# Kernel tuning notes

Hardware: AMD Instinct MI355X
Metric: run time of the kernel (lower is better)

The kernel has to match this reference:

```python
import jax, jax.numpy as jnp
import numpy as np

K = 512   # per-head dim == input dim
H = 8     # heads

def setup_inputs() -> dict:
    key = jax.random.key(0)
    ks = jax.random.split(key, 6)
    b, t = 4, 2048
    x = jax.random.normal(ks[0], (b, t, K), dtype=jnp.float32)
    s = 0.02
    Wq = jax.random.normal(ks[1], (K, K * H), dtype=jnp.float32) * s
    Wk = jax.random.normal(ks[2], (K, K * H), dtype=jnp.float32) * s
    Wv = jax.random.normal(ks[3], (K, K * H), dtype=jnp.float32) * s
    Wo = jax.random.normal(ks[4], (K * H, K), dtype=jnp.float32) * s
    bo = jnp.zeros((K,), dtype=jnp.float32)
    return {"x": x, "Wq": Wq, "Wk": Wk, "Wv": Wv, "Wo": Wo, "bo": bo}

def reference(x, Wq, Wk, Wv, Wo, bo):
    b, t, _ = x.shape
    scale = K ** 0.25
    # rearrange 'b t (k h) -> (b h) t k' == reshape (b,t,K,H) then move h next to b
    def split_heads(y):
        return y.reshape(b, t, K, H).transpose(0, 3, 1, 2)  # [b,h,t,K]
    q = split_heads(x @ Wq) / scale
    k_ = split_heads(x @ Wk) / scale
    v = split_heads(x @ Wv)
    dot = jnp.einsum('bhtk,bhsk->bhts', q, k_)      # [b,h,t,t]
    attn = jax.nn.softmax(dot, axis=-1)
    o = jnp.einsum('bhts,bhsk->bhtk', attn, v)      # [b,h,t,K]
    # '(b h) t k -> b t (h k)': heads outer in concat
    o = o.transpose(0, 2, 1, 3).reshape(b, t, H * K)
    return o @ Wo + bo
```

## Files before the change

kernel.cpp:

```cpp
#include <hip/hip_runtime.h>

typedef unsigned short u16;
typedef unsigned char u8;
typedef unsigned int u32;
typedef long i64;
typedef __attribute__((ext_vector_type(8))) short bf16x8;
typedef __attribute__((ext_vector_type(4))) float f32x4;
typedef __attribute__((ext_vector_type(16))) float f32x16;
typedef __attribute__((ext_vector_type(4))) u16 u16x4;
typedef __attribute__((ext_vector_type(4))) u32 u32x4;

__device__ __forceinline__ u16 f2bf(float f) {
  u32 u = __builtin_bit_cast(u32, f);
  return (u16)((u + 0x7FFFu + ((u >> 16) & 1u)) >> 16);
}
__device__ __forceinline__ u8 f2fp8(float f) {
  int w = __builtin_amdgcn_cvt_pk_fp8_f32(f, 0.f, 0, false);
  return (u8)(w & 0xff);
}

__device__ __forceinline__ f32x4 mfma16(bf16x8 a, bf16x8 b, f32x4 c) {
  return __builtin_amdgcn_mfma_f32_16x16x32_bf16(a, b, c, 0, 0, 0);
}
__device__ __forceinline__ f32x16 mfma32(bf16x8 a, bf16x8 b, f32x16 c) {
  return __builtin_amdgcn_mfma_f32_32x32x16_bf16(a, b, c, 0, 0, 0);
}
__device__ __forceinline__ f32x16 mfma32f8(i64 a, i64 b, f32x16 c) {
  return __builtin_amdgcn_mfma_f32_32x32x16_fp8_fp8(a, b, c, 0, 0, 0);
}

__device__ __forceinline__ void gload16(const void* g, void* l) {
  __builtin_amdgcn_global_load_lds(
      (const __attribute__((address_space(1))) unsigned int*)g,
      (__attribute__((address_space(3))) unsigned int*)l, 16, 0, 0);
}

__device__ __forceinline__ u32 cvtpk(float lo, float hi) {
  u32 r;
  asm volatile("v_cvt_pk_bf16_f32 %0, %1, %2" : "=v"(r) : "v"(lo), "v"(hi));
  return r;
}
__device__ __forceinline__ void pl32swap(u32& a, u32& b) {
  asm volatile("v_permlane32_swap_b32 %0, %1" : "+v"(a), "+v"(b));
}


__global__ void pack_x_kernel(const float* __restrict__ x, u16* __restrict__ xb) {
  const int i = blockIdx.x * 256 + threadIdx.x;
  const float4 v = ((const float4*)x)[i];
  u16x4 o;
  o[0] = f2bf(v.x); o[1] = f2bf(v.y); o[2] = f2bf(v.z); o[3] = f2bf(v.w);
  ((u16x4*)xb)[i] = o;
}

__global__ void pack_wqkv_t(const float* __restrict__ W, u16* __restrict__ Wp) {
  __shared__ u16 tile[64][72];
  const int t = threadIdx.x;
  const int c0 = blockIdx.x * 64, dd0 = blockIdx.y * 64;
#pragma unroll
  for (int s = 0; s < 4; ++s) {
    const int r = s * 16 + (t >> 4);
    const int q = (t & 15) * 4;
    const float4 v = *(const float4*)&W[(size_t)(dd0 + r) * 4096 + c0 + q];
    tile[r][q + 0] = f2bf(v.x); tile[r][q + 1] = f2bf(v.y);
    tile[r][q + 2] = f2bf(v.z); tile[r][q + 3] = f2bf(v.w);
  }
  __syncthreads();
#pragma unroll
  for (int s = 0; s < 4; ++s) {
    const int cl = s * 16 + (t >> 4);
    const int u = t & 15;
    const int cg = c0 + cl;
    const int orow = (cg & 7) * 512 + (cg >> 3);
    u16x4 o;
#pragma unroll
    for (int i = 0; i < 4; ++i) o[i] = tile[u * 4 + i][cl];
    *(u16x4*)&Wp[(size_t)orow * 512 + dd0 + u * 4] = o;
  }
}

__global__ void pack_wo_t(const float* __restrict__ W, u16* __restrict__ Wp) {
  __shared__ u16 tile[64][72];
  const int t = threadIdx.x;
  const int k0 = blockIdx.x * 64, n0 = blockIdx.y * 64;
#pragma unroll
  for (int s = 0; s < 4; ++s) {
    const int r = s * 16 + (t >> 4);
    const int q = (t & 15) * 4;
    const float4 v = *(const float4*)&W[(size_t)(k0 + r) * 512 + n0 + q];
    tile[r][q + 0] = f2bf(v.x); tile[r][q + 1] = f2bf(v.y);
    tile[r][q + 2] = f2bf(v.z); tile[r][q + 3] = f2bf(v.w);
  }
  __syncthreads();
#pragma unroll
  for (int s = 0; s < 4; ++s) {
    const int cl = s * 16 + (t >> 4);
    const int u = t & 15;
    u16x4 o;
#pragma unroll
    for (int i = 0; i < 4; ++i) o[i] = tile[u * 4 + i][cl];
    *(u16x4*)&Wp[(size_t)(n0 + cl) * 4096 + k0 + u * 4] = o;
  }
}


template <int MODE>
__global__ __launch_bounds__(256, 2) void gemm_bf16(
    const u16* __restrict__ A, const u16* __restrict__ B,
    void* __restrict__ Cout, const float* __restrict__ bias,
    int Kd, float scale) {
  __shared__ u16 Al[128 * 64];
  __shared__ u16 Bl[128 * 64];
  const int tid = threadIdx.x;
  const int lane = tid & 63;
  const int w = tid >> 6, wm = w >> 1, wn = w & 1;
  const int l15 = lane & 15, lg = lane >> 4;
  const int m0 = blockIdx.y * 128, n0 = blockIdx.x * 128;

  f32x4 acc[4][4];
  const f32x4 zero = {0.f, 0.f, 0.f, 0.f};
#pragma unroll
  for (int i = 0; i < 4; ++i)
#pragma unroll
    for (int j = 0; j < 4; ++j) acc[i][j] = zero;

  const int nk = Kd >> 6;
  for (int kt = 0; kt < nk; ++kt) {
    __syncthreads();
    const int k0 = kt << 6;
#pragma unroll
    for (int s = 0; s < 4; ++s) {
      const int chunk = s * 256 + tid;
      const int row = chunk >> 3, c = chunk & 7;
      const int cs = c ^ (row & 7);
      gload16(A + (size_t)(m0 + row) * Kd + k0 + cs * 8, &Al[chunk * 8]);
    }
#pragma unroll
    for (int s = 0; s < 4; ++s) {
      const int chunk = s * 256 + tid;
      const int row = chunk >> 3, c = chunk & 7;
      const int cs = c ^ (row & 7);
      gload16(B + (size_t)(n0 + row) * Kd + k0 + cs * 8, &Bl[chunk * 8]);
    }
    __syncthreads();
#pragma unroll
    for (int kk = 0; kk < 2; ++kk) {
      bf16x8 af[4], bfr[4];
      const int ch = kk * 4 + lg;
#pragma unroll
      for (int i = 0; i < 4; ++i) {
        const int ar = wm * 64 + i * 16 + l15;
        af[i] = *(const bf16x8*)&Al[ar * 64 + ((ch ^ (ar & 7)) * 8)];
        const int br = wn * 64 + i * 16 + l15;
        bfr[i] = *(const bf16x8*)&Bl[br * 64 + ((ch ^ (br & 7)) * 8)];
      }
#pragma unroll
      for (int i = 0; i < 4; ++i)
#pragma unroll
        for (int j = 0; j < 4; ++j)
          acc[i][j] = mfma16(af[i], bfr[j], acc[i][j]);
    }
  }

#pragma unroll
  for (int i = 0; i < 4; ++i) {
    const int gr0 = m0 + wm * 64 + i * 16 + lg * 4;
#pragma unroll
    for (int j = 0; j < 4; ++j) {
      const int gc = n0 + wn * 64 + j * 16 + l15;
      if constexpr (MODE == 0) {
        u8* O = (u8*)Cout;
        const int h = gc >> 9, d = gc & 511;
#pragma unroll
        for (int r = 0; r < 4; ++r) {
          const int grr = gr0 + r;
          const int bb = grr >> 11, t = grr & 2047;
          O[((size_t)((bb * 8 + h) * 2048 + t) << 9) + d] = f2fp8(acc[i][j][r] * scale);
        }
      } else if constexpr (MODE == 1) {
        u16* O = (u16*)Cout;
        const int h = gc >> 9, d = gc & 511;
        const int bb = gr0 >> 11, t = gr0 & 2047;
        u16x4 pk;
#pragma unroll
        for (int r = 0; r < 4; ++r) pk[r] = f2bf(acc[i][j][r]);
        *(u16x4*)&O[((size_t)((bb * 8 + h) * 512 + d) << 11) + t] = pk;
      } else {
        float* O = (float*)Cout;
        const float bv = bias[gc];
#pragma unroll
        for (int r = 0; r < 4; ++r)
          O[(size_t)(gr0 + r) * 512 + gc] = acc[i][j][r] + bv;
      }
    }
  }
}


__global__ __launch_bounds__(512, 2) void attn_kernel(
    const u8* __restrict__ Qg, const u8* __restrict__ Kg,
    const u16* __restrict__ Vtg, u16* __restrict__ Og, int nbh_pxcd) {
  __shared__ u8 K8[2][32 * 512];
  __shared__ u16 Vt_lds[2][512 * 32];
  __shared__ float Sxf[8][32][32];

  const int tid = threadIdx.x;
  const int lane = tid & 63;
  const int w = tid >> 6;
  const int pr = w >> 1, whalf = w & 1;
  const int l31 = lane & 31, hi = lane >> 5;

  const int bid = blockIdx.x;
  const int x8 = bid & 7, rest = bid >> 3;
  const int qt = rest & 15;
  const int bh = x8 * nbh_pxcd + (rest >> 4);

  const u8* Qb = Qg + (size_t)bh * 2048 * 512;
  const u8* Kb = Kg + (size_t)bh * 2048 * 512;
  const u16* Vb = Vtg + (size_t)bh * 2048 * 512;

  const int qrow = qt * 128 + pr * 32 + l31;
  i64 qf8[16];
  {
    const u8* qp = Qb + (size_t)qrow * 512 + whalf * 256 + hi * 8;
#pragma unroll
    for (int cc = 0; cc < 16; ++cc) qf8[cc] = *(const i64*)(qp + cc * 16);
  }

  f32x16 acc[8];
#pragma unroll
  for (int i = 0; i < 8; ++i) acc[i] = {};
  float m = -1e30f, lsum = 0.f;

#define STAGE_K8(tile, buf)                                                   \
  {                                                                           \
    _Pragma("unroll") for (int s_ = 0; s_ < 2; ++s_) {                        \
      const int ch = s_ * 512 + tid;                                          \
      const int row = ch >> 5, c_ = ch & 31;                                  \
      const int cs = c_ ^ row;                                                \
      gload16(Kb + (size_t)((tile) * 32 + row) * 512 + cs * 16,               \
              &K8[buf][ch * 16]);                                             \
    }                                                                         \
  }
#define STAGE_V(tile, buf)                                                    \
  {                                                                           \
    _Pragma("unroll") for (int s_ = 0; s_ < 4; ++s_) {                        \
      const int chunk = s_ * 512 + tid;                                       \
      const int row = chunk >> 2, c_ = chunk & 3;                             \
      const int cs = c_ ^ ((row >> 1) & 3);                                   \
      gload16(Vb + (size_t)row * 2048 + (tile) * 32 + cs * 8,                 \
              &Vt_lds[buf][chunk * 8]);                                       \
    }                                                                         \
  }

  STAGE_K8(0, 0);
  STAGE_V(0, 0);
  asm volatile("s_waitcnt vmcnt(0)" ::: "memory");
  __builtin_amdgcn_s_barrier();
  __builtin_amdgcn_sched_barrier(0);

  for (int step = 0; step < 64; ++step) {
    const int cur = step & 1;

    if (step < 63) {
      STAGE_K8(step + 1, cur ^ 1);
      STAGE_V(step + 1, cur ^ 1);
    }

    f32x16 st = {};
    __builtin_amdgcn_s_setprio(1);
#pragma unroll
    for (int cc = 0; cc < 16; ++cc) {
      const int g = whalf * 16 + cc;
      const int pos = g ^ l31;
      i64 kf = *(const i64*)&K8[cur][l31 * 512 + pos * 16 + hi * 8];
      st = mfma32f8(kf, qf8[cc], st);
    }
    __builtin_amdgcn_s_setprio(0);

    {
      float* sp = &Sxf[w][l31][0];
#pragma unroll
      for (int g = 0; g < 4; ++g) {
        const int slot = (2 * g + hi) ^ (l31 & 7);
        f32x4 v = {st[4 * g + 0], st[4 * g + 1], st[4 * g + 2], st[4 * g + 3]};
        *(f32x4*)&sp[slot * 4] = v;
      }
    }
    asm volatile("s_waitcnt lgkmcnt(0)" ::: "memory");
    __builtin_amdgcn_s_barrier();
    __builtin_amdgcn_sched_barrier(0);
    float s[16];
    {
      const float* sp = &Sxf[w ^ 1][l31][0];
#pragma unroll
      for (int g = 0; g < 4; ++g) {
        const int slot = (2 * g + hi) ^ (l31 & 7);
        const f32x4 v = *(const f32x4*)&sp[slot * 4];
#pragma unroll
        for (int j = 0; j < 4; ++j) s[4 * g + j] = st[4 * g + j] + v[j];
      }
    }

    float mx = s[0];
#pragma unroll
    for (int r = 1; r < 16; ++r) mx = fmaxf(mx, s[r]);
    mx = fmaxf(mx, __shfl_xor(mx, 32, 64));
    const float mnew = fmaxf(m, mx);
    if (__any(mnew > m)) {
      const float al = __expf(m - mnew);
#pragma unroll
      for (int i = 0; i < 8; ++i) acc[i] *= al;
      lsum *= al;
      m = mnew;
    }
    float p[16];
#pragma unroll
    for (int r = 0; r < 16; ++r) {
      p[r] = __expf(s[r] - m);
      lsum += p[r];
    }

    bf16x8 pf[2];
    {
      u32 wd[8];
#pragma unroll
      for (int g = 0; g < 4; ++g) {
        wd[2 * g] = cvtpk(p[4 * g + 0], p[4 * g + 1]);
        wd[2 * g + 1] = cvtpk(p[4 * g + 2], p[4 * g + 3]);
      }
      pl32swap(wd[0], wd[2]); pl32swap(wd[1], wd[3]);
      pl32swap(wd[4], wd[6]); pl32swap(wd[5], wd[7]);
      u32x4 f0 = {wd[0], wd[1], wd[2], wd[3]};
      u32x4 f1 = {wd[4], wd[5], wd[6], wd[7]};
      pf[0] = __builtin_bit_cast(bf16x8, f0);
      pf[1] = __builtin_bit_cast(bf16x8, f1);
    }

    __builtin_amdgcn_s_setprio(1);
#pragma unroll
    for (int blk = 0; blk < 8; ++blk) {
      const int drow = whalf * 256 + blk * 32 + l31;
#pragma unroll
      for (int c2 = 0; c2 < 2; ++c2) {
        const int pos = (2 * c2 + hi) ^ ((drow >> 1) & 3);
        bf16x8 vf = *(const bf16x8*)&Vt_lds[cur][drow * 32 + pos * 8];
        acc[blk] = mfma32(vf, pf[c2], acc[blk]);
      }
    }
    __builtin_amdgcn_s_setprio(0);

    asm volatile("s_waitcnt vmcnt(0)" ::: "memory");
    __builtin_amdgcn_s_barrier();
    __builtin_amdgcn_sched_barrier(0);
  }

  lsum += __shfl_xor(lsum, 32, 64);
  const float inv = 1.0f / lsum;
  const int bb = bh >> 3, h = bh & 7;
  const int tq = qt * 128 + pr * 32 + l31;
  u16* orow_p = Og + (size_t)(bb * 2048 + tq) * 4096 + h * 512;
#pragma unroll
  for (int blk = 0; blk < 8; ++blk) {
    const int dbase = whalf * 256 + blk * 32 + 4 * hi;
#pragma unroll
    for (int g = 0; g < 4; ++g) {
      u16x4 pk;
#pragma unroll
      for (int z = 0; z < 4; ++z) pk[z] = f2bf(acc[blk][4 * g + z] * inv);
      *(u16x4*)(orow_p + dbase + 8 * g) = pk;
    }
  }
#undef STAGE_K8
#undef STAGE_V
}


extern "C" void kernel_launch(void* const* d_in, const int* in_sizes, int n_in,
                              void* d_out, int out_size, void* d_ws, size_t ws_size,
                              hipStream_t stream) {
  const float* x = (const float*)d_in[0];
  const float* Wq = (const float*)d_in[1];
  const float* Wk = (const float*)d_in[2];
  const float* Wv = (const float*)d_in[3];
  const float* Wo = (const float*)d_in[4];
  const float* bo = (const float*)d_in[5];
  float* out = (float*)d_out;

  const size_t MB = 1ull << 20;
  int BB;
  if (ws_size >= 216 * MB) BB = 4;
  else if (ws_size >= 120 * MB) BB = 2;
  else BB = 1;

  char* ws = (char*)d_ws;
  u16* xb  = (u16*)(ws);
  u16* Wqp = (u16*)(ws + 8 * MB);
  u16* Wkp = (u16*)(ws + 12 * MB);
  u16* Wvp = (u16*)(ws + 16 * MB);
  u16* Wot = (u16*)(ws + 20 * MB);
  u8*  Qg  = (u8*)(ws + 24 * MB);
  u8*  Kg  = (u8*)(ws + (24 + 8 * (size_t)BB) * MB);
  u16* Vtg = (u16*)(ws + (24 + 16 * (size_t)BB) * MB);
  u16* Og  = (u16*)(ws + (24 + 32 * (size_t)BB) * MB);

  pack_x_kernel<<<dim3(4096), dim3(256), 0, stream>>>(x, xb);
  pack_wqkv_t<<<dim3(64, 8), dim3(256), 0, stream>>>(Wq, Wqp);
  pack_wqkv_t<<<dim3(64, 8), dim3(256), 0, stream>>>(Wk, Wkp);
  pack_wqkv_t<<<dim3(64, 8), dim3(256), 0, stream>>>(Wv, Wvp);
  pack_wo_t<<<dim3(64, 8), dim3(256), 0, stream>>>(Wo, Wot);

  const float qk_scale = 0.21022410381342865f;

  const int nchunk = 4 / BB;
  for (int c = 0; c < nchunk; ++c) {
    const u16* Ax = xb + (size_t)c * BB * 2048 * 512;
    gemm_bf16<0><<<dim3(32, BB * 16), dim3(256), 0, stream>>>(Ax, Wqp, (void*)Qg, nullptr, 512, qk_scale);
    gemm_bf16<0><<<dim3(32, BB * 16), dim3(256), 0, stream>>>(Ax, Wkp, (void*)Kg, nullptr, 512, qk_scale);
    gemm_bf16<1><<<dim3(32, BB * 16), dim3(256), 0, stream>>>(Ax, Wvp, (void*)Vtg, nullptr, 512, 1.0f);

    attn_kernel<<<dim3(16 * BB * 8), dim3(512), 0, stream>>>(Qg, Kg, Vtg, Og, BB);

    gemm_bf16<2><<<dim3(4, BB * 16), dim3(256), 0, stream>>>(
        Og, Wot, (void*)(out + (size_t)c * BB * 2048 * 512), bo, 4096, 1.0f);
  }
}
```

Baseline: 562.6 us.

## Software-pipeline attention: overlap softmax/PV of previous tile with QK of current

Restructures the attention loop so each iteration computes QK^T for the current K tile while running softmax and the PV MFMAs for the previous tile. V gets a triple-buffered LDS ring so the previous tile's V stays resident while the next one is staged. It also adds a lazy rescale that only updates the running max when it grows by more than 8. The aim is to hide softmax VALU latency behind matrix work, at the cost of more LDS and register pressure.

```diff
diff --git a/kernel.cpp b/kernel.cpp
--- a/kernel.cpp
+++ b/kernel.cpp
@@ -201,7 +201,7 @@
     const u8* __restrict__ Qg, const u8* __restrict__ Kg,
     const u16* __restrict__ Vtg, u16* __restrict__ Og, int nbh_pxcd) {
   __shared__ u8 K8[2][32 * 512];
-  __shared__ u16 Vt_lds[2][512 * 32];
+  __shared__ u16 V3[3][512 * 32];
   __shared__ float Sxf[8][32][32];
 
   const int tid = threadIdx.x;
@@ -231,6 +231,8 @@
 #pragma unroll
   for (int i = 0; i < 8; ++i) acc[i] = {};
   float m = -1e30f, lsum = 0.f;
+  f32x16 sprev;
+  bf16x8 pf0, pf1;
 
 #define STAGE_K8(tile, buf)                                                   \
   {                                                                           \
@@ -249,7 +251,49 @@
       const int row = chunk >> 2, c_ = chunk & 3;                             \
       const int cs = c_ ^ ((row >> 1) & 3);                                   \
       gload16(Vb + (size_t)row * 2048 + (tile) * 32 + cs * 8,                 \
-              &Vt_lds[buf][chunk * 8]);                                       \
+              &V3[buf][chunk * 8]);                                           \
+    }                                                                         \
+  }
+
+#define SM_PREV()                                                             \
+  {                                                                           \
+    float mx = sprev[0];                                                      \
+    _Pragma("unroll") for (int r = 1; r < 16; ++r) mx = fmaxf(mx, sprev[r]);  \
+    mx = fmaxf(mx, __shfl_xor(mx, 32, 64));                                   \
+    if (!__all(mx - m <= 8.0f)) {                                             \
+      const float mnew = fmaxf(m, mx);                                        \
+      const float al = __expf(m - mnew);                                      \
+      _Pragma("unroll") for (int z = 0; z < 8; ++z) acc[z] *= al;             \
+      lsum *= al;                                                             \
+      m = mnew;                                                               \
+    }                                                                         \
+    _Pragma("unroll") for (int r = 0; r < 16; ++r) {                          \
+      sprev[r] = __expf(sprev[r] - m);                                        \
+      lsum += sprev[r];                                                       \
+    }                                                                         \
+    u32 wd[8];                                                                \
+    _Pragma("unroll") for (int g = 0; g < 4; ++g) {                           \
+      wd[2 * g] = cvtpk(sprev[4 * g + 0], sprev[4 * g + 1]);                  \
+      wd[2 * g + 1] = cvtpk(sprev[4 * g + 2], sprev[4 * g + 3]);              \
+    }                                                                         \
+    pl32swap(wd[0], wd[2]); pl32swap(wd[1], wd[3]);                           \
+    pl32swap(wd[4], wd[6]); pl32swap(wd[5], wd[7]);                           \
+    u32x4 f0_ = {wd[0], wd[1], wd[2], wd[3]};                                 \
+    u32x4 f1_ = {wd[4], wd[5], wd[6], wd[7]};                                 \
+    pf0 = __builtin_bit_cast(bf16x8, f0_);                                    \
+    pf1 = __builtin_bit_cast(bf16x8, f1_);                                    \
+  }
+
+#define PV_PREV(buf)                                                          \
+  {                                                                           \
+    _Pragma("unroll") for (int blk = 0; blk < 8; ++blk) {                     \
+      const int drow = whalf * 256 + blk * 32 + l31;                          \
+      const int pos0 = hi ^ ((drow >> 1) & 3);                                \
+      const int pos1 = (2 + hi) ^ ((drow >> 1) & 3);                          \
+      bf16x8 v0 = *(const bf16x8*)&V3[buf][drow * 32 + pos0 * 8];             \
+      bf16x8 v1 = *(const bf16x8*)&V3[buf][drow * 32 + pos1 * 8];             \
+      acc[blk] = mfma32(v0, pf0, acc[blk]);                                   \
+      acc[blk] = mfma32(v1, pf1, acc[blk]);                                   \
     }                                                                         \
   }
 
@@ -259,12 +303,15 @@
   __builtin_amdgcn_s_barrier();
   __builtin_amdgcn_sched_barrier(0);
 
-  for (int step = 0; step < 64; ++step) {
-    const int cur = step & 1;
-
-    if (step < 63) {
-      STAGE_K8(step + 1, cur ^ 1);
-      STAGE_V(step + 1, cur ^ 1);
+  int vw = 1;
+  int vr = 2;
+
+  for (int t = 0; t < 64; ++t) {
+    const int kb = t & 1;
+
+    if (t < 63) {
+      STAGE_K8(t + 1, kb ^ 1);
+      STAGE_V(t + 1, vw);
     }
 
     f32x16 st = {};
@@ -273,10 +320,12 @@
     for (int cc = 0; cc < 16; ++cc) {
       const int g = whalf * 16 + cc;
       const int pos = g ^ l31;
-      i64 kf = *(const i64*)&K8[cur][l31 * 512 + pos * 16 + hi * 8];
+      i64 kf = *(const i64*)&K8[kb][l31 * 512 + pos * 16 + hi * 8];
       st = mfma32f8(kf, qf8[cc], st);
     }
     __builtin_amdgcn_s_setprio(0);
+
+    if (t > 0) SM_PREV();
 
     {
       float* sp = &Sxf[w][l31][0];
@@ -290,7 +339,7 @@
     asm volatile("s_waitcnt lgkmcnt(0)" ::: "memory");
     __builtin_amdgcn_s_barrier();
     __builtin_amdgcn_sched_barrier(0);
-    float s[16];
+
     {
       const float* sp = &Sxf[w ^ 1][l31][0];
 #pragma unroll
@@ -298,62 +347,26 @@
         const int slot = (2 * g + hi) ^ (l31 & 7);
         const f32x4 v = *(const f32x4*)&sp[slot * 4];
 #pragma unroll
-        for (int j = 0; j < 4; ++j) s[4 * g + j] = st[4 * g + j] + v[j];
+        for (int j = 0; j < 4; ++j) st[4 * g + j] += v[j];
       }
     }
-
-    float mx = s[0];
-#pragma unroll
-    for (int r = 1; r < 16; ++r) mx = fmaxf(mx, s[r]);
-    mx = fmaxf(mx, __shfl_xor(mx, 32, 64));
-    const float mnew = fmaxf(m, mx);
-    if (__any(mnew > m)) {
-      const float al = __expf(m - mnew);
-#pragma unroll
-      for (int i = 0; i < 8; ++i) acc[i] *= al;
-      lsum *= al;
-      m = mnew;
-    }
-    float p[16];
-#pragma unroll
-    for (int r = 0; r < 16; ++r) {
-      p[r] = __expf(s[r] - m);
-      lsum += p[r];
-    }
-
-    bf16x8 pf[2];
-    {
-      u32 wd[8];
-#pragma unroll
-      for (int g = 0; g < 4; ++g) {
-        wd[2 * g] = cvtpk(p[4 * g + 0], p[4 * g + 1]);
-        wd[2 * g + 1] = cvtpk(p[4 * g + 2], p[4 * g + 3]);
-      }
-      pl32swap(wd[0], wd[2]); pl32swap(wd[1], wd[3]);
-      pl32swap(wd[4], wd[6]); pl32swap(wd[5], wd[7]);
-      u32x4 f0 = {wd[0], wd[1], wd[2], wd[3]};
-      u32x4 f1 = {wd[4], wd[5], wd[6], wd[7]};
-      pf[0] = __builtin_bit_cast(bf16x8, f0);
-      pf[1] = __builtin_bit_cast(bf16x8, f1);
-    }
-
-    __builtin_amdgcn_s_setprio(1);
-#pragma unroll
-    for (int blk = 0; blk < 8; ++blk) {
-      const int drow = whalf * 256 + blk * 32 + l31;
-#pragma unroll
-      for (int c2 = 0; c2 < 2; ++c2) {
-        const int pos = (2 * c2 + hi) ^ ((drow >> 1) & 3);
-        bf16x8 vf = *(const bf16x8*)&Vt_lds[cur][drow * 32 + pos * 8];
-        acc[blk] = mfma32(vf, pf[c2], acc[blk]);
-      }
-    }
-    __builtin_amdgcn_s_setprio(0);
+    if (t > 0) {
+      __builtin_amdgcn_s_setprio(1);
+      PV_PREV(vr);
+      __builtin_amdgcn_s_setprio(0);
+    }
+    sprev = st;
 
     asm volatile("s_waitcnt vmcnt(0)" ::: "memory");
     __builtin_amdgcn_s_barrier();
     __builtin_amdgcn_sched_barrier(0);
-  }
+
+    vw = (vw == 2) ? 0 : vw + 1;
+    vr = (vr == 2) ? 0 : vr + 1;
+  }
+
+  SM_PREV();
+  PV_PREV(vr);
 
   lsum += __shfl_xor(lsum, 32, 64);
   const float inv = 1.0f / lsum;
@@ -373,6 +386,8 @@
   }
 #undef STAGE_K8
 #undef STAGE_V
+#undef SM_PREV
+#undef PV_PREV
 }
 
 
```

Measured after the change: 576.1 us. +2.4%, slower.
